# Performance work log

Measured on AMD Instinct MI355X. Metric: run time of the kernel, lower is better.

Reference implementation:

```python
import jax, jax.numpy as jnp
from jax import lax
import numpy as np

B, CIN, COUT, H, W = 4, 64, 64, 128, 128
K = 3      # kernel size
G = 1      # groups (== offset groups)
PAD = 1
STRIDE = 1


def setup_inputs() -> dict:
    key = jax.random.key(0)
    k1, k2, k3 = jax.random.split(key, 3)
    x = jax.random.normal(k1, (B, CIN, H, W), jnp.float32)
    # offset-predicting conv weight: (2*G*K*K, CIN, K, K); small init like real nets
    w_offset = jax.random.normal(k2, (2 * G * K * K, CIN, K, K), jnp.float32) * 0.01
    # deformable conv weight: (COUT, CIN//G, K, K)
    w_deform = jax.random.normal(k3, (COUT, CIN // G, K, K), jnp.float32) * (1.0 / np.sqrt(CIN * K * K))
    return {"x": x, "w_offset": w_offset, "w_deform": w_deform}


def _deform_conv2d(x, w_offset, w_deform):
    Bn, C, Hi, Wi = x.shape
    K2 = K * K
    Cg = C // G
    # 1) predict offsets with a plain conv
    offset = lax.conv_general_dilated(
        x, w_offset, (STRIDE, STRIDE), [(PAD, PAD), (PAD, PAD)],
        dimension_numbers=("NCHW", "OIHW", "NCHW"))
    Ho, Wo = offset.shape[2], offset.shape[3]
    # torchvision layout: channel 2*(g*K2 + i*K + j) = dy, +1 = dx
    off = offset.reshape(Bn, G, K2, 2, Ho, Wo)
    dy = off[:, :, :, 0]  # (B,G,K2,Ho,Wo)
    dx = off[:, :, :, 1]
    # base sampling grid
    ky = jnp.repeat(jnp.arange(K), K).astype(x.dtype)  # (K2,) kernel row offsets
    kx = jnp.tile(jnp.arange(K), K).astype(x.dtype)    # (K2,) kernel col offsets
    base_y = (jnp.arange(Ho) * STRIDE - PAD).astype(x.dtype)[:, None]   # (Ho,1)
    base_x = (jnp.arange(Wo) * STRIDE - PAD).astype(x.dtype)[None, :]   # (1,Wo)
    py = base_y[None, None, None] + ky[None, None, :, None, None] + dy  # (B,G,K2,Ho,Wo)
    px = base_x[None, None, None] + kx[None, None, :, None, None] + dx
    # 2) bilinear sampling with zero padding outside the image
    y0 = jnp.floor(py)
    x0 = jnp.floor(px)
    ly = py - y0
    lx = px - x0
    y0i = y0.astype(jnp.int32)
    x0i = x0.astype(jnp.int32)
    xr = x.reshape(Bn, G, Cg, Hi, Wi)

    def corner(yi, xi, wgt):
        valid = ((yi >= 0) & (yi < Hi) & (xi >= 0) & (xi < Wi)).astype(x.dtype)
        yc = jnp.clip(yi, 0, Hi - 1)
        xc = jnp.clip(xi, 0, Wi - 1)
        # gather per (batch, group): xg[:, yy, xx] -> (Cg, K2, Ho, Wo)
        g = jax.vmap(jax.vmap(lambda xg, yy, xx: xg[:, yy, xx]))(xr, yc, xc)
        return g * (wgt * valid)[:, :, None]  # broadcast over Cg

    v = (corner(y0i,     x0i,     (1 - ly) * (1 - lx))
         + corner(y0i,     x0i + 1, (1 - ly) * lx)
         + corner(y0i + 1, x0i,     ly * (1 - lx))
         + corner(y0i + 1, x0i + 1, ly * lx))  # (B,G,Cg,K2,Ho,Wo)
    # 3) grouped contraction with the deformable conv weight
    wr = w_deform.reshape(G, COUT // G, Cg, K2)
    out = jnp.einsum('bgckhw,gock->bgohw', v, wr)
    return out.reshape(Bn, COUT, Ho, Wo)


def reference(x, w_offset, w_deform):
    return _deform_conv2d(x, w_offset, w_deform)
```

## Files before the change

### kernel.cpp

```cpp
#include <hip/hip_runtime.h>

#define B_    4
#define CIN_  64
#define COUT_ 64
#define H_    128
#define W_    128
#define HW_   (H_*W_)
#define K2_   9
#define NOFF_ 18

#define PR_   132
#define PC_   136
#define TROWS 5
#define TCOLS 70
#define NSEG  (TROWS * 8 * TCOLS)
#define NSEGP 2816

typedef _Float16 f16x8 __attribute__((ext_vector_type(8)));
typedef float    f32x4 __attribute__((ext_vector_type(4)));

__device__ __forceinline__ f16x8 splat8(float f) {
    _Float16 h = (_Float16)f;
    return (f16x8){h, h, h, h, h, h, h, h};
}

#define NW_B   (COUT_ * 576)
#define NW_OB  (32 * 576)
#define NBORD  (4 * 12544)
__global__ __launch_bounds__(256) void x2h_prep(const float* __restrict__ x,
                                                const float* __restrict__ wd,
                                                const float* __restrict__ wo,
                                                _Float16* __restrict__ hx,
                                                _Float16* __restrict__ wt_b,
                                                _Float16* __restrict__ wt_ob) {
    const int blk = blockIdx.x;
    const int b = blk >> 7, y = blk & 127;
    const int xp = threadIdx.x & 127;
    const int ch = threadIdx.x >> 7;
    const float* xs = x + ((b * CIN_ + ch * 32) * H_ + y) * W_ + xp;
    _Float16* hd = hx + (((size_t)b * PR_ + y + 2) * PC_ + xp + 3) * 64 + ch * 32;

    f16x8 h[4];
    #pragma unroll
    for (int j = 0; j < 4; ++j)
        #pragma unroll
        for (int t = 0; t < 8; ++t)
            h[j][t] = (_Float16)xs[(j * 8 + t) * HW_];
    #pragma unroll
    for (int j = 0; j < 4; ++j)
        *(f16x8*)(hd + j * 8) = h[j];

    const int gid = blk * 256 + threadIdx.x;
    if (gid < NW_B) {
        int blk512 = gid >> 9, w = gid & 511;
        int nl = w >> 5, cc = w & 31;
        int kb = blk512 & 1, t = blk512 >> 1;
        int mb = t / 9, k2 = t - 9 * mb;
        int o = mb * 16 + nl, c = kb * 32 + cc;
        wt_b[gid] = (_Float16)wd[(o * CIN_ + c) * K2_ + k2];
    } else if (gid < NW_B + NW_OB) {
        int u = gid - NW_B;
        int blk512 = u >> 9, w = u & 511;
        int nl = w >> 5, cc = w & 31;
        int kb = blk512 & 1, t = blk512 >> 1;
        int mt = t / 9, k2 = t - 9 * mt;
        int oc = mt * 16 + nl, c = kb * 32 + cc;
        wt_ob[u] = (_Float16)((oc < NOFF_) ? wo[(oc * CIN_ + c) * K2_ + k2] : 0.f);
    } else if (gid < NW_B + NW_OB + NBORD) {
        int s = gid - (NW_B + NW_OB);
        int b2 = s / 12544, u = s % 12544;
        int cs = u & 7, cell = u >> 3;
        int r, c;
        if (cell < 544) {
            int r4 = cell / 136; c = cell % 136;
            r = (r4 < 2) ? r4 : r4 + 128;
        } else {
            int c2 = cell - 544;
            r = 2 + (c2 >> 3);
            int c8 = c2 & 7;
            c = (c8 < 3) ? c8 : c8 + 128;
        }
        *(f16x8*)(hx + (((size_t)b2 * PR_ + r) * PC_ + c) * 64 + cs * 8) = splat8(0.f);
    }
}

__global__ __launch_bounds__(256, 3) void deform_all(const _Float16* __restrict__ hx,
                                                     const _Float16* __restrict__ wt_b,
                                                     const _Float16* __restrict__ wt_ob,
                                                     float* __restrict__ out) {
    __shared__ __align__(16) _Float16 xt[NSEGP * 8];

    const int tid = threadIdx.x;
    int blk = blockIdx.x;
    blk = (blk & 7) * 128 + (blk >> 3);
    const int b   = blk >> 8;
    const int r2  = blk & 255;
    const int oh  = r2 >> 1;
    const int ow0 = (r2 & 1) << 6;

    const _Float16* hrow = hx + (((size_t)b * PR_ + oh) * PC_ + ow0) * 64;
    #pragma unroll
    for (int t = 0; t < NSEGP / 256; ++t) {
        int d  = t * 256 + tid;
        int dc = min(d, NSEG - 1);
        int col = dc % TCOLS;
        int rc  = dc / TCOLS;
        int cs  = rc & 7;
        int r   = rc >> 3;
        const _Float16* src = hrow + ((size_t)r * PC_ + col) * 64 + cs * 8;
        __builtin_amdgcn_global_load_lds(
            (const __attribute__((address_space(1))) void*)src,
            (__attribute__((address_space(3))) void*)(xt + (size_t)d * 8),
            16, 0, 0);
    }
    __syncthreads();

    const int lane = tid & 63;
    const int cq   = tid >> 6;
    const int quad = lane >> 4;
    const int nl   = lane & 15;
    const int pix  = cq * 16 + nl;
    const int ow   = ow0 + pix;

    const _Float16* wob_l = wt_ob + nl * 32 + quad * 8;
    const _Float16* wtb_l = wt_b  + nl * 32 + quad * 8;

    f32x4 oacc[2];
    oacc[0] = (f32x4){0.f, 0.f, 0.f, 0.f};
    oacc[1] = (f32x4){0.f, 0.f, 0.f, 0.f};
    #pragma unroll
    for (int t9 = 0; t9 < 9; ++t9) {
        int ky = t9 / 3, kx = t9 - 3 * (t9 / 3);
        #pragma unroll
        for (int kb = 0; kb < 2; ++kb) {
            f16x8 bfr = *(const f16x8*)&xt[((((ky + 1) * 8) + kb * 4 + quad) * TCOLS + pix + kx + 2) * 8];
            #pragma unroll
            for (int mt = 0; mt < 2; ++mt) {
                f16x8 afr = *(const f16x8*)(wob_l + (((mt * 9 + t9) * 2 + kb) << 9));
                oacc[mt] = __builtin_amdgcn_mfma_f32_16x16x32_f16(afr, bfr, oacc[mt], 0, 0, 0);
            }
        }
    }

    float dyv[9], dxv[9];
    #pragma unroll
    for (int k2 = 0; k2 < 9; ++k2) {
        const int oc0 = 2 * k2;
        const int mt  = oc0 >> 4;
        const int sq  = (oc0 & 15) >> 2;
        const int r0  = oc0 & 3;
        dyv[k2] = __shfl(oacc[mt][r0],     sq * 16 + nl, 64);
        dxv[k2] = __shfl(oacc[mt][r0 + 1], sq * 16 + nl, 64);
    }

    f32x4 acc[4];
    #pragma unroll
    for (int mb = 0; mb < 4; ++mb) acc[mb] = (f32x4){0.f, 0.f, 0.f, 0.f};

    #pragma unroll
    for (int k2 = 0; k2 < 9; ++k2) {
        const int ky = k2 / 3, kx = k2 - 3 * (k2 / 3);
        float py = (float)(oh - 1 + ky) + dyv[k2];
        float px = (float)(ow - 1 + kx) + dxv[k2];
        float y0f = floorf(py), x0f = floorf(px);
        float ly = py - y0f,    lx = px - x0f;
        int   y0 = (int)y0f,    x0 = (int)x0f;
        int   y1 = y0 + 1,      x1 = x0 + 1;

        float wy0 = 1.f - ly, wx0 = 1.f - lx;
        float w00 = wy0 * wx0, w01 = wy0 * lx, w10 = ly * wx0, w11 = ly * lx;

        bool vy0 = (unsigned)y0 < (unsigned)H_;
        bool vy1 = (unsigned)y1 < (unsigned)H_;
        bool vx0 = (unsigned)x0 < (unsigned)W_;
        bool vx1 = (unsigned)x1 < (unsigned)W_;
        if (!(vy0 & vx0)) w00 = 0.f;
        if (!(vy0 & vx1)) w01 = 0.f;
        if (!(vy1 & vx0)) w10 = 0.f;
        if (!(vy1 & vx1)) w11 = 0.f;

        f16x8 W00 = splat8(w00), W01 = splat8(w01), W10 = splat8(w10), W11 = splat8(w11);

        int ty0 = y0 - (oh - 2), ty1 = y1 - (oh - 2);
        int tx0 = x0 - (ow0 - 3), tx1 = x1 - (ow0 - 3);
        bool i00 = (unsigned)ty0 < TROWS && (unsigned)tx0 < TCOLS;
        bool i01 = (unsigned)ty0 < TROWS && (unsigned)tx1 < TCOLS;
        bool i10 = (unsigned)ty1 < TROWS && (unsigned)tx0 < TCOLS;
        bool i11 = (unsigned)ty1 < TROWS && (unsigned)tx1 < TCOLS;
        bool ok = (w00 == 0.f || i00) && (w01 == 0.f || i01) &&
                  (w10 == 0.f || i10) && (w11 == 0.f || i11);

        f16x8 v0, v1;
        if (ok) {
            int tyc0 = min(max(ty0, 0), TROWS - 1), tyc1 = min(max(ty1, 0), TROWS - 1);
            int txc0 = min(max(tx0, 0), TCOLS - 1), txc1 = min(max(tx1, 0), TCOLS - 1);
            int a00 = ((tyc0 * 8 + quad) * TCOLS + txc0) * 8;
            int a01 = ((tyc0 * 8 + quad) * TCOLS + txc1) * 8;
            int a10 = ((tyc1 * 8 + quad) * TCOLS + txc0) * 8;
            int a11 = ((tyc1 * 8 + quad) * TCOLS + txc1) * 8;
            const int KB1 = 4 * TCOLS * 8;
            f16x8 c00a = *(const f16x8*)&xt[a00], c00b = *(const f16x8*)&xt[a00 + KB1];
            f16x8 c01a = *(const f16x8*)&xt[a01], c01b = *(const f16x8*)&xt[a01 + KB1];
            f16x8 c10a = *(const f16x8*)&xt[a10], c10b = *(const f16x8*)&xt[a10 + KB1];
            f16x8 c11a = *(const f16x8*)&xt[a11], c11b = *(const f16x8*)&xt[a11 + KB1];
            v0 = c00a * W00 + c01a * W01 + c10a * W10 + c11a * W11;
            v1 = c00b * W00 + c01b * W01 + c10b * W10 + c11b * W11;
        } else {
            int y0c = min(max(y0, 0), H_ - 1), y1c = min(max(y1, 0), H_ - 1);
            int x0c = min(max(x0, 0), W_ - 1), x1c = min(max(x1, 0), W_ - 1);
            const _Float16* hb = hx + (size_t)b * PR_ * PC_ * 64 + quad * 8;
            const _Float16* g00 = hb + (((y0c + 2) * PC_) + x0c + 3) * 64;
            const _Float16* g01 = hb + (((y0c + 2) * PC_) + x1c + 3) * 64;
            const _Float16* g10 = hb + (((y1c + 2) * PC_) + x0c + 3) * 64;
            const _Float16* g11 = hb + (((y1c + 2) * PC_) + x1c + 3) * 64;
            v0 = (*(const f16x8*)g00) * W00 + (*(const f16x8*)g01) * W01 +
                 (*(const f16x8*)g10) * W10 + (*(const f16x8*)g11) * W11;
            v1 = (*(const f16x8*)(g00 + 32)) * W00 + (*(const f16x8*)(g01 + 32)) * W01 +
                 (*(const f16x8*)(g10 + 32)) * W10 + (*(const f16x8*)(g11 + 32)) * W11;
        }

        #pragma unroll
        for (int mb = 0; mb < 4; ++mb) {
            f16x8 afr0 = *(const f16x8*)(wtb_l + (((mb * 9 + k2) * 2 + 0) << 9));
            acc[mb] = __builtin_amdgcn_mfma_f32_16x16x32_f16(afr0, v0, acc[mb], 0, 0, 0);
            f16x8 afr1 = *(const f16x8*)(wtb_l + (((mb * 9 + k2) * 2 + 1) << 9));
            acc[mb] = __builtin_amdgcn_mfma_f32_16x16x32_f16(afr1, v1, acc[mb], 0, 0, 0);
        }
    }

    #pragma unroll
    for (int mb = 0; mb < 4; ++mb)
        #pragma unroll
        for (int r = 0; r < 4; ++r) {
            int o = mb * 16 + quad * 4 + r;
            out[(b * COUT_ + o) * HW_ + oh * W_ + ow0 + pix] = acc[mb][r];
        }
}

extern "C" void kernel_launch(void* const* d_in, const int* in_sizes, int n_in,
                              void* d_out, int out_size, void* d_ws, size_t ws_size,
                              hipStream_t stream) {
    const float* x        = (const float*)d_in[0];
    const float* w_offset = (const float*)d_in[1];
    const float* w_deform = (const float*)d_in[2];
    float* out = (float*)d_out;

    _Float16* hx    = (_Float16*)d_ws;
    _Float16* wt_b  = hx + (size_t)B_ * PR_ * PC_ * 64;
    _Float16* wt_ob = wt_b + (size_t)NW_B;

    x2h_prep<<<B_ * H_, 256, 0, stream>>>(x, w_deform, w_offset, hx, wt_b, wt_ob);
    deform_all<<<B_ * H_ * (W_ / 64), 256, 0, stream>>>(hx, wt_b, wt_ob, out);
}
```

Baseline: 113.5 us.

## Precompute bilinear tap addresses and weights, hoist weight-fragment loads, raise MFMA priority

Splits the per-tap loop into a precompute pass that stores the bilinear corner weights, the base LDS address and the in-tile and dx/dy bitmasks for all 9 taps, then a second pass that does the gathers and MFMAs. Inside the MFMA pass, all weight fragments for a tap are loaded before the sample gather, and the MFMA block is wrapped in s_setprio so matrix work gets scheduling priority. The aim is to shorten the dependency chain between address math, LDS loads and MFMAs and to let loads overlap compute. In exchange it raises register pressure from the 9x4 weight array and 9 addresses, which could lower occupancy.

```diff
diff --git a/kernel.cpp b/kernel.cpp
--- a/kernel.cpp
+++ b/kernel.cpp
@@ -153,10 +153,9 @@
         dxv[k2] = __shfl(oacc[mt][r0 + 1], sq * 16 + nl, 64);
     }
 
-    f32x4 acc[4];
-    #pragma unroll
-    for (int mb = 0; mb < 4; ++mb) acc[mb] = (f32x4){0.f, 0.f, 0.f, 0.f};
-
+    int   A00[9];
+    float Wf[9][4];
+    unsigned okm = 0, dxm = 0, dym = 0;
     #pragma unroll
     for (int k2 = 0; k2 < 9; ++k2) {
         const int ky = k2 / 3, kx = k2 - 3 * (k2 / 3);
@@ -178,26 +177,47 @@
         if (!(vy0 & vx1)) w01 = 0.f;
         if (!(vy1 & vx0)) w10 = 0.f;
         if (!(vy1 & vx1)) w11 = 0.f;
-
-        f16x8 W00 = splat8(w00), W01 = splat8(w01), W10 = splat8(w10), W11 = splat8(w11);
-
-        int ty0 = y0 - (oh - 2), ty1 = y1 - (oh - 2);
-        int tx0 = x0 - (ow0 - 3), tx1 = x1 - (ow0 - 3);
+        Wf[k2][0] = w00; Wf[k2][1] = w01; Wf[k2][2] = w10; Wf[k2][3] = w11;
+
+        int ty0 = y0 - (oh - 2), ty1 = ty0 + 1;
+        int tx0 = x0 - (ow0 - 3), tx1 = tx0 + 1;
         bool i00 = (unsigned)ty0 < TROWS && (unsigned)tx0 < TCOLS;
         bool i01 = (unsigned)ty0 < TROWS && (unsigned)tx1 < TCOLS;
         bool i10 = (unsigned)ty1 < TROWS && (unsigned)tx0 < TCOLS;
         bool i11 = (unsigned)ty1 < TROWS && (unsigned)tx1 < TCOLS;
         bool ok = (w00 == 0.f || i00) && (w01 == 0.f || i01) &&
                   (w10 == 0.f || i10) && (w11 == 0.f || i11);
+        if (ok) okm |= 1u << k2;
+
+        int tyc0 = min(max(ty0, 0), TROWS - 1), tyc1 = min(max(ty1, 0), TROWS - 1);
+        int txc0 = min(max(tx0, 0), TCOLS - 1), txc1 = min(max(tx1, 0), TCOLS - 1);
+        if (txc1 != txc0) dxm |= 1u << k2;
+        if (tyc1 != tyc0) dym |= 1u << k2;
+        A00[k2] = ((tyc0 * 8 + quad) * TCOLS + txc0) * 8;
+    }
+
+    f32x4 acc[4];
+    #pragma unroll
+    for (int mb = 0; mb < 4; ++mb) acc[mb] = (f32x4){0.f, 0.f, 0.f, 0.f};
+
+    #pragma unroll
+    for (int k2 = 0; k2 < 9; ++k2) {
+        f16x8 afr0[4], afr1[4];
+        #pragma unroll
+        for (int mb = 0; mb < 4; ++mb) {
+            afr0[mb] = *(const f16x8*)(wtb_l + (((mb * 9 + k2) * 2 + 0) << 9));
+            afr1[mb] = *(const f16x8*)(wtb_l + (((mb * 9 + k2) * 2 + 1) << 9));
+        }
+
+        f16x8 W00 = splat8(Wf[k2][0]), W01 = splat8(Wf[k2][1]);
+        f16x8 W10 = splat8(Wf[k2][2]), W11 = splat8(Wf[k2][3]);
 
         f16x8 v0, v1;
-        if (ok) {
-            int tyc0 = min(max(ty0, 0), TROWS - 1), tyc1 = min(max(ty1, 0), TROWS - 1);
-            int txc0 = min(max(tx0, 0), TCOLS - 1), txc1 = min(max(tx1, 0), TCOLS - 1);
-            int a00 = ((tyc0 * 8 + quad) * TCOLS + txc0) * 8;
-            int a01 = ((tyc0 * 8 + quad) * TCOLS + txc1) * 8;
-            int a10 = ((tyc1 * 8 + quad) * TCOLS + txc0) * 8;
-            int a11 = ((tyc1 * 8 + quad) * TCOLS + txc1) * 8;
+        if (okm & (1u << k2)) {
+            const int a00 = A00[k2];
+            const int a01 = a00 + (int)((dxm >> k2) & 1u) * 8;
+            const int a10 = a00 + (int)((dym >> k2) & 1u) * (8 * TCOLS * 8);
+            const int a11 = a10 + (a01 - a00);
             const int KB1 = 4 * TCOLS * 8;
             f16x8 c00a = *(const f16x8*)&xt[a00], c00b = *(const f16x8*)&xt[a00 + KB1];
             f16x8 c01a = *(const f16x8*)&xt[a01], c01b = *(const f16x8*)&xt[a01 + KB1];
@@ -206,8 +226,12 @@
             v0 = c00a * W00 + c01a * W01 + c10a * W10 + c11a * W11;
             v1 = c00b * W00 + c01b * W01 + c10b * W10 + c11b * W11;
         } else {
-            int y0c = min(max(y0, 0), H_ - 1), y1c = min(max(y1, 0), H_ - 1);
-            int x0c = min(max(x0, 0), W_ - 1), x1c = min(max(x1, 0), W_ - 1);
+            const int ky = k2 / 3, kx = k2 - 3 * (k2 / 3);
+            float py = (float)(oh - 1 + ky) + dyv[k2];
+            float px = (float)(ow - 1 + kx) + dxv[k2];
+            int y0 = (int)floorf(py), x0 = (int)floorf(px);
+            int y0c = min(max(y0, 0), H_ - 1), y1c = min(max(y0 + 1, 0), H_ - 1);
+            int x0c = min(max(x0, 0), W_ - 1), x1c = min(max(x0 + 1, 0), W_ - 1);
             const _Float16* hb = hx + (size_t)b * PR_ * PC_ * 64 + quad * 8;
             const _Float16* g00 = hb + (((y0c + 2) * PC_) + x0c + 3) * 64;
             const _Float16* g01 = hb + (((y0c + 2) * PC_) + x1c + 3) * 64;
@@ -219,13 +243,13 @@
                  (*(const f16x8*)(g10 + 32)) * W10 + (*(const f16x8*)(g11 + 32)) * W11;
         }
 
+        __builtin_amdgcn_s_setprio(1);
         #pragma unroll
         for (int mb = 0; mb < 4; ++mb) {
-            f16x8 afr0 = *(const f16x8*)(wtb_l + (((mb * 9 + k2) * 2 + 0) << 9));
-            acc[mb] = __builtin_amdgcn_mfma_f32_16x16x32_f16(afr0, v0, acc[mb], 0, 0, 0);
-            f16x8 afr1 = *(const f16x8*)(wtb_l + (((mb * 9 + k2) * 2 + 1) << 9));
-            acc[mb] = __builtin_amdgcn_mfma_f32_16x16x32_f16(afr1, v1, acc[mb], 0, 0, 0);
-        }
+            acc[mb] = __builtin_amdgcn_mfma_f32_16x16x32_f16(afr0[mb], v0, acc[mb], 0, 0, 0);
+            acc[mb] = __builtin_amdgcn_mfma_f32_16x16x32_f16(afr1[mb], v1, acc[mb], 0, 0, 0);
+        }
+        __builtin_amdgcn_s_setprio(0);
     }
 
     #pragma unroll
```

Result: faster. 110.0 us (median of 2 runs) (-3.1%).
